# Kernel optimization log

Hardware: AMD Instinct MI355X
Metric: run time of the kernel (lower is better)

The kernel has to match this reference:

```python
import jax, jax.numpy as jnp
import numpy as np

LATENT = 3
HIDDEN = 16
INP = LATENT + 1  # prev_z cat action
B = 1048576


def setup_inputs() -> dict:
    key = jax.random.key(0)
    ks = jax.random.split(key, 11)
    s_ih = 1.0 / np.sqrt(HIDDEN)
    return {
        "prev_z": jax.random.normal(ks[0], (B, LATENT), jnp.float32),
        "action": jax.random.normal(ks[1], (B, 1), jnp.float32),
        "prev_h": jax.random.normal(ks[2], (B, HIDDEN), jnp.float32),
        # GRUCell params (torch layout: [3*H, in] and [3*H, H], gate order r,z,n)
        "W_ih": jax.random.uniform(ks[3], (3 * HIDDEN, INP), jnp.float32, -s_ih, s_ih),
        "W_hh": jax.random.uniform(ks[4], (3 * HIDDEN, HIDDEN), jnp.float32, -s_ih, s_ih),
        "b_ih": jax.random.uniform(ks[5], (3 * HIDDEN,), jnp.float32, -s_ih, s_ih),
        "b_hh": jax.random.uniform(ks[6], (3 * HIDDEN,), jnp.float32, -s_ih, s_ih),
        # prior heads
        "W_mu": jax.random.uniform(ks[7], (LATENT, HIDDEN), jnp.float32, -s_ih, s_ih),
        "b_mu": jax.random.uniform(ks[8], (LATENT,), jnp.float32, -s_ih, s_ih),
        "W_lv": jax.random.uniform(ks[9], (LATENT, HIDDEN), jnp.float32, -s_ih, s_ih),
        "b_lv": jax.random.uniform(ks[10], (LATENT,), jnp.float32, -s_ih, s_ih),
    }


def reference(prev_z, action, prev_h, W_ih, W_hh, b_ih, b_hh, W_mu, b_mu, W_lv, b_lv):
    x = jnp.concatenate([prev_z, action], axis=-1)              # [B, 4]
    gi = x @ W_ih.T + b_ih                                       # [B, 3H]
    gh = prev_h @ W_hh.T + b_hh                                  # [B, 3H]
    i_r, i_z, i_n = jnp.split(gi, 3, axis=-1)
    h_r, h_z, h_n = jnp.split(gh, 3, axis=-1)
    r = jax.nn.sigmoid(i_r + h_r)
    z = jax.nn.sigmoid(i_z + h_z)
    n = jnp.tanh(i_n + r * h_n)
    h = (1.0 - z) * n + z * prev_h                               # [B, H]
    mu = h @ W_mu.T + b_mu                                       # [B, 3]
    logvar = jnp.clip(h @ W_lv.T + b_lv, -5.0, 5.0)              # [B, 3]
    return mu, logvar, h
```

## Files before the change

kernel.cpp:

```cpp
#include <hip/hip_runtime.h>

#define TPB 64
#define WPT 4
#define ROW_DW 20
#define LDS_ROW_F32 (64 * ROW_DW)
#define LDS_MU_F32 192
#define LDS_WAVE_F32 (LDS_ROW_F32 + 2 * LDS_MU_F32)
#define LOG2E 1.44269504088896340736f

typedef _Float16 half8 __attribute__((ext_vector_type(8)));
typedef __fp16  fp16x2 __attribute__((ext_vector_type(2)));
typedef float f32x4 __attribute__((ext_vector_type(4)));

__device__ __forceinline__ half8 pack8(float4 lo, float4 hi) {
    union { fp16x2 p[4]; half8 h; } u;
    u.p[0] = __builtin_amdgcn_cvt_pkrtz(lo.x, lo.y);
    u.p[1] = __builtin_amdgcn_cvt_pkrtz(lo.z, lo.w);
    u.p[2] = __builtin_amdgcn_cvt_pkrtz(hi.x, hi.y);
    u.p[3] = __builtin_amdgcn_cvt_pkrtz(hi.z, hi.w);
    return u.h;
}


__global__ __launch_bounds__(64) void prep_kernel(
    const float* __restrict__ W_ih, const float* __restrict__ W_hh,
    const float* __restrict__ b_ih, const float* __restrict__ b_hh,
    const float* __restrict__ W_mu, const float* __restrict__ b_mu,
    const float* __restrict__ W_lv, const float* __restrict__ b_lv,
    void* __restrict__ wsv)
{
    _Float16* wsB = (_Float16*)wsv;
    const int l = threadIdx.x;
    const int col = l & 15, kg = l >> 4;

    #pragma unroll
    for (int t = 0; t < 4; ++t) {
        const int gate = (t == 0) ? col : (t == 1) ? (16 + col) : (32 + col);
        const float scale = (t <= 1) ? -LOG2E : -2.0f * LOG2E;
        #pragma unroll
        for (int i = 0; i < 8; ++i) {
            const int k = kg * 8 + i;
            float v = 0.f;
            if (t <= 1) {
                if (k < 4)       v = W_ih[gate * 4 + k];
                else if (k < 20) v = W_hh[gate * 16 + (k - 4)];
            } else if (t == 2) {
                if (k < 4)       v = W_ih[gate * 4 + k];
            } else {
                if (k >= 4 && k < 20) v = W_hh[gate * 16 + (k - 4)];
            }
            wsB[t * 512 + l * 8 + i] = (_Float16)(v * scale);
        }
    }
    #pragma unroll
    for (int i = 0; i < 8; ++i) {
        const int k = kg * 8 + i;
        wsB[4 * 512 + l * 8 + i] = (_Float16)((k == col + 4) ? 1.f : 0.f);
    }
    #pragma unroll
    for (int i = 0; i < 8; ++i) {
        const int k = kg * 8 + i;
        const int m = col;
        float v = 0.f;
        if (m < 3) {
            if (k < 16)       v = W_mu[m * 16 + k];
            else if (k == 20) v = b_mu[m];
        } else if (m < 6) {
            if (k < 16)       v = W_lv[(m - 3) * 16 + k];
            else if (k == 20) v = b_lv[m - 3];
        }
        wsB[5 * 512 + l * 8 + i] = (_Float16)v;
    }
    if (l < 16) {
        float4* b4 = (float4*)((char*)wsv + 6144);
        b4[l] = make_float4(-LOG2E * (b_ih[l] + b_hh[l]),
                            -LOG2E * (b_ih[16 + l] + b_hh[16 + l]),
                            -2.0f * LOG2E * b_ih[32 + l],
                            -2.0f * LOG2E * b_hh[32 + l]);
    }
}

template<bool EXACT>
__global__ __launch_bounds__(TPB, 4) void rssm_kernel(
    const float* __restrict__ prev_z,
    const float* __restrict__ action,
    const float* __restrict__ prev_h,
    const void*  __restrict__ wsv,
    float* __restrict__ out_mu,
    float* __restrict__ out_lv,
    float* __restrict__ out_h,
    int B)
{
    __shared__ float Wl[LDS_WAVE_F32];
    const int lane = threadIdx.x;
    const int col = lane & 15, kg = lane >> 4;
    const int wbase = blockIdx.x * 64;
    if (!EXACT && wbase >= B) return;

    float* W  = Wl;
    float* MU = W + LDS_ROW_F32;
    float* LV = MU + LDS_MU_F32;

    const half8* Bp = (const half8*)wsv;
    const half8 bR  = Bp[lane];
    const half8 bZ  = Bp[64 + lane];
    const half8 bNi = Bp[128 + lane];
    const half8 bNh = Bp[192 + lane];
    const half8 bHp = Bp[256 + lane];
    const half8 a2  = Bp[320 + lane];
    const float4 bias = ((const float4*)((const char*)wsv + 6144))[col];

    {
        const float4* hg = (const float4*)prev_h;
        #pragma unroll
        for (int i = 0; i < 4; ++i) {
            const int fi = i * 64 + lane;
            const int r = fi >> 2, w = fi & 3;
            const int gi = EXACT ? (wbase * 4 + fi) : min(wbase * 4 + fi, B * 4 - 1);
            const float4 v = hg[gi];
            *(float4*)&W[r * ROW_DW + 4 + w * 4] = v;
        }
        const int zr = EXACT ? (wbase + lane) : min(wbase + lane, B - 1);
        const float z0 = prev_z[zr * 3 + 0];
        const float z1 = prev_z[zr * 3 + 1];
        const float z2 = prev_z[zr * 3 + 2];
        const float ac = action[zr];
        *(float4*)&W[lane * ROW_DW] = make_float4(z0, z1, z2, ac);
    }

    #pragma unroll
    for (int t = 0; t < WPT; ++t) {
        const float* ap = &W[(t * 16 + col) * ROW_DW + kg * 8];
        const float4 z4 = make_float4(0.f, 0.f, 0.f, 0.f);
        const float4 p0 = (kg < 3) ? *(const float4*)ap : z4;
        const float4 p1 = (kg < 2) ? *(const float4*)(ap + 4) : z4;
        const half8 a = pack8(p0, p1);

        f32x4 accR  = {bias.x, bias.x, bias.x, bias.x};
        f32x4 accZ  = {bias.y, bias.y, bias.y, bias.y};
        f32x4 accNi = {bias.z, bias.z, bias.z, bias.z};
        f32x4 accNh = {bias.w, bias.w, bias.w, bias.w};
        f32x4 accHp = {0.f, 0.f, 0.f, 0.f};
        accR  = __builtin_amdgcn_mfma_f32_16x16x32_f16(a, bR,  accR,  0, 0, 0);
        accZ  = __builtin_amdgcn_mfma_f32_16x16x32_f16(a, bZ,  accZ,  0, 0, 0);
        accNi = __builtin_amdgcn_mfma_f32_16x16x32_f16(a, bNi, accNi, 0, 0, 0);
        accNh = __builtin_amdgcn_mfma_f32_16x16x32_f16(a, bNh, accNh, 0, 0, 0);
        accHp = __builtin_amdgcn_mfma_f32_16x16x32_f16(a, bHp, accHp, 0, 0, 0);

        #pragma unroll
        for (int q = 0; q < 4; ++q) {
            const float r  = __builtin_amdgcn_rcpf(1.0f + __builtin_amdgcn_exp2f(accR[q]));
            const float z  = __builtin_amdgcn_rcpf(1.0f + __builtin_amdgcn_exp2f(accZ[q]));
            const float ta = fmaf(r, accNh[q], accNi[q]);
            const float n  = fmaf(2.0f,
                                  __builtin_amdgcn_rcpf(1.0f + __builtin_amdgcn_exp2f(ta)),
                                  -1.0f);
            const float hv = fmaf(z, accHp[q] - n, n);
            W[(t * 16 + kg * 4 + q) * ROW_DW + 4 + col] = hv;
        }

        half8 b2;
        if (kg < 2) {
            const float* hr = &W[(t * 16 + col) * ROW_DW + 4 + kg * 8];
            b2 = pack8(*(const float4*)hr, *(const float4*)(hr + 4));
        } else {
            #pragma unroll
            for (int i = 0; i < 8; ++i) b2[i] = (_Float16)0.f;
            if (kg == 2) b2[4] = (_Float16)1.0f;
        }
        f32x4 acc2 = {0.f, 0.f, 0.f, 0.f};
        acc2 = __builtin_amdgcn_mfma_f32_16x16x32_f16(a2, b2, acc2, 0, 0, 0);

        const int mr = (t * 16 + col) * 3;
        if (kg == 0) {
            MU[mr + 0] = acc2[0];
            MU[mr + 1] = acc2[1];
            MU[mr + 2] = acc2[2];
            LV[mr + 0] = fminf(fmaxf(acc2[3], -5.0f), 5.0f);
        } else if (kg == 1) {
            LV[mr + 1] = fminf(fmaxf(acc2[0], -5.0f), 5.0f);
            LV[mr + 2] = fminf(fmaxf(acc2[1], -5.0f), 5.0f);
        }

        {
            const int r = lane >> 2, w = lane & 3;
            const float4 hv4 = *(const float4*)&W[(t * 16 + r) * ROW_DW + 4 + w * 4];
            const int orow = wbase + t * 16 + r;
            if (EXACT || orow < B)
                *(float4*)&out_h[(size_t)orow * 16 + w * 4] = hv4;
        }
    }

    if (lane < 48) {
        const int gi = wbase * 3 + lane * 4;
        if (EXACT || gi + 3 < B * 3) {
            *(float4*)&out_mu[gi] = *(const float4*)&MU[lane * 4];
            *(float4*)&out_lv[gi] = *(const float4*)&LV[lane * 4];
        }
    }
}

extern "C" void kernel_launch(void* const* d_in, const int* in_sizes, int n_in,
                              void* d_out, int out_size, void* d_ws, size_t ws_size,
                              hipStream_t stream) {
    const float* prev_z = (const float*)d_in[0];
    const float* action = (const float*)d_in[1];
    const float* prev_h = (const float*)d_in[2];
    const float* W_ih   = (const float*)d_in[3];
    const float* W_hh   = (const float*)d_in[4];
    const float* b_ih   = (const float*)d_in[5];
    const float* b_hh   = (const float*)d_in[6];
    const float* W_mu   = (const float*)d_in[7];
    const float* b_mu   = (const float*)d_in[8];
    const float* W_lv   = (const float*)d_in[9];
    const float* b_lv   = (const float*)d_in[10];

    const int B = in_sizes[0] / 3;
    float* out    = (float*)d_out;
    float* out_mu = out;
    float* out_lv = out + (size_t)3 * B;
    float* out_h  = out + (size_t)6 * B;

    prep_kernel<<<1, 64, 0, stream>>>(W_ih, W_hh, b_ih, b_hh,
                                      W_mu, b_mu, W_lv, b_lv, d_ws);

    const int rows_per_block = 64;
    const int blocks = (B + rows_per_block - 1) / rows_per_block;
    if ((B % rows_per_block) == 0)
        rssm_kernel<true><<<blocks, TPB, 0, stream>>>(prev_z, action, prev_h, d_ws,
                                                      out_mu, out_lv, out_h, B);
    else
        rssm_kernel<false><<<blocks, TPB, 0, stream>>>(prev_z, action, prev_h, d_ws,
                                                       out_mu, out_lv, out_h, B);
}
```

Before: 41.76 us.

## Process two row chunks per block with register prefetch of the second chunk

Each 64-thread block now handles 128 rows as two chunks. The second chunk's prev_h, prev_z and action are loaded into registers before the first chunk is computed, so global load latency overlaps with MFMA work, and the per-block weight fragment loads are amortized over twice as many rows. The second chunk uses its own double-buffered LDS, which doubles LDS use per block, and launch_bounds is raised to 6 blocks per CU. The grid shrinks by half, which trades launch-level parallelism for this in-block latency hiding.

Result: slower. 51.62 us (+23.6%).

```diff
diff --git a/kernel.cpp b/kernel.cpp
--- a/kernel.cpp
+++ b/kernel.cpp
@@ -5,7 +5,6 @@
 #define ROW_DW 20
 #define LDS_ROW_F32 (64 * ROW_DW)
 #define LDS_MU_F32 192
-#define LDS_WAVE_F32 (LDS_ROW_F32 + 2 * LDS_MU_F32)
 #define LOG2E 1.44269504088896340736f
 
 typedef _Float16 half8 __attribute__((ext_vector_type(8)));
@@ -80,54 +79,13 @@
     }
 }
 
-template<bool EXACT>
-__global__ __launch_bounds__(TPB, 4) void rssm_kernel(
-    const float* __restrict__ prev_z,
-    const float* __restrict__ action,
-    const float* __restrict__ prev_h,
-    const void*  __restrict__ wsv,
-    float* __restrict__ out_mu,
-    float* __restrict__ out_lv,
-    float* __restrict__ out_h,
-    int B)
+__device__ __forceinline__ void compute_chunk(
+    float* __restrict__ W, float* __restrict__ MU, float* __restrict__ LV,
+    half8 bR, half8 bZ, half8 bNi, half8 bNh, half8 bHp, half8 a2, float4 bias,
+    int col, int kg, int lane, int wbase, int B, bool exact,
+    float* __restrict__ out_mu, float* __restrict__ out_lv,
+    float* __restrict__ out_h)
 {
-    __shared__ float Wl[LDS_WAVE_F32];
-    const int lane = threadIdx.x;
-    const int col = lane & 15, kg = lane >> 4;
-    const int wbase = blockIdx.x * 64;
-    if (!EXACT && wbase >= B) return;
-
-    float* W  = Wl;
-    float* MU = W + LDS_ROW_F32;
-    float* LV = MU + LDS_MU_F32;
-
-    const half8* Bp = (const half8*)wsv;
-    const half8 bR  = Bp[lane];
-    const half8 bZ  = Bp[64 + lane];
-    const half8 bNi = Bp[128 + lane];
-    const half8 bNh = Bp[192 + lane];
-    const half8 bHp = Bp[256 + lane];
-    const half8 a2  = Bp[320 + lane];
-    const float4 bias = ((const float4*)((const char*)wsv + 6144))[col];
-
-    {
-        const float4* hg = (const float4*)prev_h;
-        #pragma unroll
-        for (int i = 0; i < 4; ++i) {
-            const int fi = i * 64 + lane;
-            const int r = fi >> 2, w = fi & 3;
-            const int gi = EXACT ? (wbase * 4 + fi) : min(wbase * 4 + fi, B * 4 - 1);
-            const float4 v = hg[gi];
-            *(float4*)&W[r * ROW_DW + 4 + w * 4] = v;
-        }
-        const int zr = EXACT ? (wbase + lane) : min(wbase + lane, B - 1);
-        const float z0 = prev_z[zr * 3 + 0];
-        const float z1 = prev_z[zr * 3 + 1];
-        const float z2 = prev_z[zr * 3 + 2];
-        const float ac = action[zr];
-        *(float4*)&W[lane * ROW_DW] = make_float4(z0, z1, z2, ac);
-    }
-
     #pragma unroll
     for (int t = 0; t < WPT; ++t) {
         const float* ap = &W[(t * 16 + col) * ROW_DW + kg * 8];
@@ -186,17 +144,100 @@
             const int r = lane >> 2, w = lane & 3;
             const float4 hv4 = *(const float4*)&W[(t * 16 + r) * ROW_DW + 4 + w * 4];
             const int orow = wbase + t * 16 + r;
-            if (EXACT || orow < B)
+            if (exact || orow < B)
                 *(float4*)&out_h[(size_t)orow * 16 + w * 4] = hv4;
         }
     }
 
     if (lane < 48) {
         const int gi = wbase * 3 + lane * 4;
-        if (EXACT || gi + 3 < B * 3) {
+        if (exact || gi + 3 < B * 3) {
             *(float4*)&out_mu[gi] = *(const float4*)&MU[lane * 4];
             *(float4*)&out_lv[gi] = *(const float4*)&LV[lane * 4];
         }
+    }
+}
+
+template<bool EXACT>
+__global__ __launch_bounds__(TPB, 6) void rssm_kernel(
+    const float* __restrict__ prev_z,
+    const float* __restrict__ action,
+    const float* __restrict__ prev_h,
+    const void*  __restrict__ wsv,
+    float* __restrict__ out_mu,
+    float* __restrict__ out_lv,
+    float* __restrict__ out_h,
+    int B)
+{
+    __shared__ float Wl[2][LDS_ROW_F32];
+    __shared__ float MUl[2][LDS_MU_F32];
+    __shared__ float LVl[2][LDS_MU_F32];
+    const int lane = threadIdx.x;
+    const int col = lane & 15, kg = lane >> 4;
+    const int bbase = blockIdx.x * 128;
+    if (!EXACT && bbase >= B) return;
+
+    const half8* Bp = (const half8*)wsv;
+    const half8 bR  = Bp[lane];
+    const half8 bZ  = Bp[64 + lane];
+    const half8 bNi = Bp[128 + lane];
+    const half8 bNh = Bp[192 + lane];
+    const half8 bHp = Bp[256 + lane];
+    const half8 a2  = Bp[320 + lane];
+    const float4 bias = ((const float4*)((const char*)wsv + 6144))[col];
+
+    const float4* hg = (const float4*)prev_h;
+
+    float4 hreg[4], xar;
+    {
+        const int cb4 = bbase * 4;
+        #pragma unroll
+        for (int i = 0; i < 4; ++i) {
+            const int gi = EXACT ? (cb4 + i * 64 + lane)
+                                 : min(cb4 + i * 64 + lane, B * 4 - 1);
+            hreg[i] = hg[gi];
+        }
+        const int zr = EXACT ? (bbase + lane) : min(bbase + lane, B - 1);
+        xar = make_float4(prev_z[zr * 3 + 0], prev_z[zr * 3 + 1],
+                          prev_z[zr * 3 + 2], action[zr]);
+    }
+    #pragma unroll
+    for (int i = 0; i < 4; ++i) {
+        const int fi = i * 64 + lane;
+        const int r = fi >> 2, w = fi & 3;
+        *(float4*)&Wl[0][r * ROW_DW + 4 + w * 4] = hreg[i];
+    }
+    *(float4*)&Wl[0][lane * ROW_DW] = xar;
+
+    const int c1base = bbase + 64;
+    const bool have_c1 = EXACT || (c1base < B);
+    if (have_c1) {
+        const int cb4 = c1base * 4;
+        #pragma unroll
+        for (int i = 0; i < 4; ++i) {
+            const int gi = EXACT ? (cb4 + i * 64 + lane)
+                                 : min(cb4 + i * 64 + lane, B * 4 - 1);
+            hreg[i] = hg[gi];
+        }
+        const int zr = EXACT ? (c1base + lane) : min(c1base + lane, B - 1);
+        xar = make_float4(prev_z[zr * 3 + 0], prev_z[zr * 3 + 1],
+                          prev_z[zr * 3 + 2], action[zr]);
+    }
+
+    compute_chunk(Wl[0], MUl[0], LVl[0], bR, bZ, bNi, bNh, bHp, a2, bias,
+                  col, kg, lane, bbase, B, EXACT, out_mu, out_lv, out_h);
+
+    if (have_c1) {
+        #pragma unroll
+        for (int i = 0; i < 4; ++i) {
+            const int fi = i * 64 + lane;
+            const int r = fi >> 2, w = fi & 3;
+            *(float4*)&Wl[1][r * ROW_DW + 4 + w * 4] = hreg[i];
+        }
+        *(float4*)&Wl[1][lane * ROW_DW] = xar;
+
+        compute_chunk(Wl[1], MUl[1], LVl[1], bR, bZ, bNi, bNh, bHp, a2, bias,
+                      col, kg, lane, c1base, B, EXACT, out_mu, out_lv, out_h);
     }
 }
 
@@ -224,7 +265,7 @@
     prep_kernel<<<1, 64, 0, stream>>>(W_ih, W_hh, b_ih, b_hh,
                                       W_mu, b_mu, W_lv, b_lv, d_ws);
 
-    const int rows_per_block = 64;
+    const int rows_per_block = 128;
     const int blocks = (B + rows_per_block - 1) / rows_per_block;
     if ((B % rows_per_block) == 0)
         rssm_kernel<true><<<blocks, TPB, 0, stream>>>(prev_z, action, prev_h, d_ws,
```
